# Kernel tuning notes

Hardware: AMD Instinct MI355X
Metric: run time of the kernel (lower is better)

Reference implementation:

```python
import jax, jax.numpy as jnp
import numpy as np

FH = FW = 3

def _decomp_layer(x, f0, f1, f2, f3):
    # x: (B, C, H, W); f0: (F, r), f1: (FH, r), f2: (FW, r), f3: (C, r)
    B, C, H, W = x.shape
    Ho, Wo = H - FH + 1, W - FW + 1
    # unfold -> patches (B, C, Ho, Wo, FH, FW); fixed 3x3 loop, not a data-dim loop
    patches = jnp.stack(
        [jnp.stack([x[:, :, i:i + Ho, j:j + Wo] for j in range(FW)], axis=-1)
         for i in range(FH)], axis=-2)
    # permute to (B, Ho, Wo, FH, FW, C) as in torch's permute(0,2,3,4,5,1)
    patches = patches.transpose(0, 2, 3, 4, 5, 1)
    # CP contraction: collapse fh, fw, c against rank factors, then expand to filters
    t = jnp.einsum('bhwxyc,xr,yr,cr->bhwr', patches, f1, f2, f3)
    return jnp.einsum('bhwr,fr->bfhw', t, f0)  # (B, F, Ho, Wo)


def setup_inputs() -> dict:
    key = jax.random.key(0)
    ks = jax.random.split(key, 12)
    B, C, H, W = 512, 3, 32, 32
    F, R, NC = 32, 16, 10
    s = 0.1
    return {
        'x': jax.random.normal(ks[0], (B, C, H, W), jnp.float32),
        'l1_f0': jax.random.normal(ks[1], (F, R), jnp.float32) * s,
        'l1_f1': jax.random.normal(ks[2], (FH, R), jnp.float32) * s,
        'l1_f2': jax.random.normal(ks[3], (FW, R), jnp.float32) * s,
        'l1_f3': jax.random.normal(ks[4], (C, R), jnp.float32) * s,
        'l2_f0': jax.random.normal(ks[5], (F, R), jnp.float32) * s,
        'l2_f1': jax.random.normal(ks[6], (FH, R), jnp.float32) * s,
        'l2_f2': jax.random.normal(ks[7], (FW, R), jnp.float32) * s,
        'l2_f3': jax.random.normal(ks[8], (F, R), jnp.float32) * s,
        'W_cls': jax.random.normal(ks[9], (NC, 25088), jnp.float32) * 0.01,
        'b_cls': jnp.zeros((NC,), jnp.float32),
    }


def reference(x, l1_f0, l1_f1, l1_f2, l1_f3, l2_f0, l2_f1, l2_f2, l2_f3, W_cls, b_cls):
    h = _decomp_layer(x, l1_f0, l1_f1, l1_f2, l1_f3)        # (B, 32, 30, 30)
    h = _decomp_layer(h, l2_f0, l2_f1, l2_f2, l2_f3)        # (B, 32, 28, 28)
    h = h.reshape(h.shape[0], -1)                            # (B, 25088)
    logits = h @ W_cls.T + b_cls
    return jax.nn.log_softmax(logits, axis=1)
```

## Files before the change

### kernel.cpp

```cpp
#include <hip/hip_runtime.h>
#include <math.h>


__global__ __launch_bounds__(256) void precomp1(
    const float* __restrict__ l1_f0, const float* __restrict__ l1_f1,
    const float* __restrict__ l1_f2, const float* __restrict__ l1_f3,
    const float* __restrict__ l2_f0, const float* __restrict__ l2_f1,
    const float* __restrict__ l2_f2, const float* __restrict__ l2_f3,
    const float* __restrict__ Wcls,
    float* __restrict__ Wc3, float* __restrict__ Kc) {
    __shared__ float sWc2[784];
    __shared__ float sM[256];
    const int tid = threadIdx.x;
    const int blk = blockIdx.x;

    if (blk < 160) {
        const int n = blk >> 4, r2 = blk & 15;
        for (int q = tid; q < 784; q += 256) {
            float acc = 0.f;
#pragma unroll
            for (int f = 0; f < 32; ++f)
                acc += l2_f0[f * 16 + r2] * Wcls[n * 25088 + f * 784 + q];
            sWc2[q] = acc;
        }
        __syncthreads();
        float cw[9];
#pragma unroll
        for (int ij = 0; ij < 9; ++ij) {
            int i = ij / 3, j = ij - (ij / 3) * 3;
            cw[ij] = l2_f1[i * 16 + r2] * l2_f2[j * 16 + r2];
        }
        for (int p = tid; p < 900; p += 256) {
            int h = p / 30, w = p - (p / 30) * 30;
            float acc = 0.f;
#pragma unroll
            for (int i = 0; i < 3; ++i) {
                int hh = h - i;
                if (hh < 0 || hh > 27) continue;
#pragma unroll
                for (int j = 0; j < 3; ++j) {
                    int ww = w - j;
                    if (ww < 0 || ww > 27) continue;
                    acc += cw[i * 3 + j] * sWc2[hh * 28 + ww];
                }
            }
            Wc3[blk * 900 + p] = acc;
        }
    } else {
        {
            int r1 = tid >> 4, r2 = tid & 15;
            float acc = 0.f;
#pragma unroll
            for (int f = 0; f < 32; ++f)
                acc += l1_f0[f * 16 + r1] * l2_f3[f * 16 + r2];
            sM[tid] = acc;
        }
        __syncthreads();
        for (int t = tid; t < 432; t += 256) {
            int c = t / 144;
            int rem = t - c * 144;
            int ij = rem >> 4;
            int r2 = rem & 15;
            int i = ij / 3, j = ij - i * 3;
            float acc = 0.f;
#pragma unroll
            for (int r1 = 0; r1 < 16; ++r1) {
                float cw1v = l1_f1[i * 16 + r1] * l1_f2[j * 16 + r1];
                acc += l1_f3[c * 16 + r1] * cw1v * sM[r1 * 16 + r2];
            }
            Kc[t] = acc;
        }
    }
}

__global__ __launch_bounds__(256) void precomp2(
    const float* __restrict__ Wc3, const float* __restrict__ Kc,
    float* __restrict__ Wx) {
    const int t = blockIdx.x * 256 + threadIdx.x;
    if (t >= 30720) return;
    const int n = t / 3072;
    const int rem = t - n * 3072;
    const int c = rem >> 10;
    const int p = rem & 1023;
    const int H = p >> 5, W = p & 31;
    const float* wn = Wc3 + n * 14400;
    float acc = 0.f;
#pragma unroll
    for (int i = 0; i < 3; ++i) {
        int hh = H - i;
        if (hh < 0 || hh >= 30) continue;
#pragma unroll
        for (int j = 0; j < 3; ++j) {
            int ww = W - j;
            if (ww < 0 || ww >= 30) continue;
            const float* wp = wn + hh * 30 + ww;
            const float* kp = Kc + (c * 9 + i * 3 + j) * 16;
#pragma unroll
            for (int r2 = 0; r2 < 16; ++r2)
                acc += kp[r2] * wp[r2 * 900];
        }
    }
    Wx[t] = acc;
}

__global__ __launch_bounds__(256) void cls_kernel(
    const float* __restrict__ x, const float* __restrict__ Wx,
    const float* __restrict__ b_cls, float* __restrict__ out) {
    __shared__ float sred[4][10];
    __shared__ float slog[10];
    const int tid = threadIdx.x;
    const int b = blockIdx.x;
    const float4* xb = (const float4*)(x + b * 3072);
    const float4* wx4 = (const float4*)Wx;

    float acc[10];
#pragma unroll
    for (int n = 0; n < 10; ++n) acc[n] = 0.f;
#pragma unroll
    for (int k = 0; k < 3; ++k) {
        const int idx = tid + k * 256;
        float4 xv = xb[idx];
#pragma unroll
        for (int n = 0; n < 10; ++n) {
            float4 wv = wx4[n * 768 + idx];
            acc[n] += xv.x * wv.x + xv.y * wv.y + xv.z * wv.z + xv.w * wv.w;
        }
    }

    const int lane = tid & 63, wid = tid >> 6;
#pragma unroll
    for (int n = 0; n < 10; ++n) {
        float v = acc[n];
        for (int off = 32; off > 0; off >>= 1)
            v += __shfl_down(v, off, 64);
        if (lane == 0) sred[wid][n] = v;
    }
    __syncthreads();
    if (tid < 10) {
        slog[tid] = b_cls[tid] + sred[0][tid] + sred[1][tid]
                  + sred[2][tid] + sred[3][tid];
    }
    __syncthreads();
    if (tid < 10) {
        float m = -1e30f;
#pragma unroll
        for (int n = 0; n < 10; ++n) m = fmaxf(m, slog[n]);
        float ssum = 0.f;
#pragma unroll
        for (int n = 0; n < 10; ++n) ssum += expf(slog[n] - m);
        out[b * 10 + tid] = slog[tid] - m - logf(ssum);
    }
}

extern "C" void kernel_launch(void* const* d_in, const int* in_sizes, int n_in,
                              void* d_out, int out_size, void* d_ws, size_t ws_size,
                              hipStream_t stream) {
    const float* x     = (const float*)d_in[0];
    const float* l1_f0 = (const float*)d_in[1];
    const float* l1_f1 = (const float*)d_in[2];
    const float* l1_f2 = (const float*)d_in[3];
    const float* l1_f3 = (const float*)d_in[4];
    const float* l2_f0 = (const float*)d_in[5];
    const float* l2_f1 = (const float*)d_in[6];
    const float* l2_f2 = (const float*)d_in[7];
    const float* l2_f3 = (const float*)d_in[8];
    const float* Wcls  = (const float*)d_in[9];
    const float* bcls  = (const float*)d_in[10];
    float* out = (float*)d_out;

    float* Wc3 = (float*)d_ws;
    float* Kc  = Wc3 + 144000;
    float* Wx  = Kc + 432;

    precomp1<<<dim3(161), dim3(256), 0, stream>>>(
        l1_f0, l1_f1, l1_f2, l1_f3, l2_f0, l2_f1, l2_f2, l2_f3, Wcls, Wc3, Kc);
    precomp2<<<dim3(120), dim3(256), 0, stream>>>(Wc3, Kc, Wx);
    cls_kernel<<<dim3(512), dim3(256), 0, stream>>>(x, Wx, bcls, out);
}
```

Baseline: 93.04 us.

## Fold both conv layers into a combined 5x5 kernel and merge precompute kernels

Replaces the two precompute kernels with one. Each block redundantly builds the composed layer1∘layer2 weight tensor G (C×5×5×F) in shared memory, then correlates W_cls directly with that 5x5 kernel to produce Wx. This removes one kernel launch and the global round trip through the Wc3 and Kc intermediates. In exchange every block recomputes the small factor products, and each output now does 25×32 taps instead of 9×16.

```diff
diff --git a/kernel.cpp b/kernel.cpp
--- a/kernel.cpp
+++ b/kernel.cpp
@@ -2,102 +2,92 @@
 #include <math.h>
 
 
-__global__ __launch_bounds__(256) void precomp1(
+__global__ __launch_bounds__(256) void wx_kernel(
     const float* __restrict__ l1_f0, const float* __restrict__ l1_f1,
     const float* __restrict__ l1_f2, const float* __restrict__ l1_f3,
     const float* __restrict__ l2_f0, const float* __restrict__ l2_f1,
     const float* __restrict__ l2_f2, const float* __restrict__ l2_f3,
     const float* __restrict__ Wcls,
-    float* __restrict__ Wc3, float* __restrict__ Kc) {
-    __shared__ float sWc2[784];
+    float* __restrict__ Wx) {
     __shared__ float sM[256];
+    __shared__ float sK[432];
+    __shared__ float sE[1200];
+    __shared__ float sG[2400];
     const int tid = threadIdx.x;
-    const int blk = blockIdx.x;
 
-    if (blk < 160) {
-        const int n = blk >> 4, r2 = blk & 15;
-        for (int q = tid; q < 784; q += 256) {
-            float acc = 0.f;
+    {
+        int r1 = tid >> 4, r2 = tid & 15;
+        float acc = 0.f;
 #pragma unroll
-            for (int f = 0; f < 32; ++f)
-                acc += l2_f0[f * 16 + r2] * Wcls[n * 25088 + f * 784 + q];
-            sWc2[q] = acc;
+        for (int f = 0; f < 32; ++f)
+            acc += l1_f0[f * 16 + r1] * l2_f3[f * 16 + r2];
+        sM[tid] = acc;
+    }
+    __syncthreads();
+    for (int t = tid; t < 432; t += 256) {
+        int r2 = t & 15;
+        int e = t >> 4;
+        int c = e / 9, ij = e - c * 9;
+        int i = ij / 3, j = ij - i * 3;
+        float acc = 0.f;
+#pragma unroll
+        for (int r1 = 0; r1 < 16; ++r1)
+            acc += l1_f3[c * 16 + r1] * l1_f1[i * 16 + r1] * l1_f2[j * 16 + r1]
+                 * sM[r1 * 16 + r2];
+        sK[t] = acc;
+    }
+    __syncthreads();
+    for (int t = tid; t < 1200; t += 256) {
+        int r2 = t & 15;
+        int e = t >> 4;
+        int c = e / 25, uv = e - c * 25;
+        int u = uv / 5, v = uv - u * 5;
+        float acc = 0.f;
+        int ilo = u > 2 ? u - 2 : 0, ihi = u < 2 ? u : 2;
+        int jlo = v > 2 ? v - 2 : 0, jhi = v < 2 ? v : 2;
+        for (int i = ilo; i <= ihi; ++i) {
+            int k = u - i;
+            for (int j = jlo; j <= jhi; ++j) {
+                int l = v - j;
+                acc += sK[(c * 9 + i * 3 + j) * 16 + r2]
+                     * l2_f1[k * 16 + r2] * l2_f2[l * 16 + r2];
+            }
         }
-        __syncthreads();
-        float cw[9];
+        sE[t] = acc;
+    }
+    __syncthreads();
+    for (int t = tid; t < 2400; t += 256) {
+        int f = t & 31;
+        int e = t >> 5;
+        float acc = 0.f;
 #pragma unroll
-        for (int ij = 0; ij < 9; ++ij) {
-            int i = ij / 3, j = ij - (ij / 3) * 3;
-            cw[ij] = l2_f1[i * 16 + r2] * l2_f2[j * 16 + r2];
-        }
-        for (int p = tid; p < 900; p += 256) {
-            int h = p / 30, w = p - (p / 30) * 30;
-            float acc = 0.f;
-#pragma unroll
-            for (int i = 0; i < 3; ++i) {
-                int hh = h - i;
-                if (hh < 0 || hh > 27) continue;
-#pragma unroll
-                for (int j = 0; j < 3; ++j) {
-                    int ww = w - j;
-                    if (ww < 0 || ww > 27) continue;
-                    acc += cw[i * 3 + j] * sWc2[hh * 28 + ww];
-                }
-            }
-            Wc3[blk * 900 + p] = acc;
-        }
-    } else {
-        {
-            int r1 = tid >> 4, r2 = tid & 15;
-            float acc = 0.f;
-#pragma unroll
-            for (int f = 0; f < 32; ++f)
-                acc += l1_f0[f * 16 + r1] * l2_f3[f * 16 + r2];
-            sM[tid] = acc;
-        }
-        __syncthreads();
-        for (int t = tid; t < 432; t += 256) {
-            int c = t / 144;
-            int rem = t - c * 144;
-            int ij = rem >> 4;
-            int r2 = rem & 15;
-            int i = ij / 3, j = ij - i * 3;
-            float acc = 0.f;
-#pragma unroll
-            for (int r1 = 0; r1 < 16; ++r1) {
-                float cw1v = l1_f1[i * 16 + r1] * l1_f2[j * 16 + r1];
-                acc += l1_f3[c * 16 + r1] * cw1v * sM[r1 * 16 + r2];
-            }
-            Kc[t] = acc;
-        }
+        for (int r2 = 0; r2 < 16; ++r2)
+            acc += sE[e * 16 + r2] * l2_f0[f * 16 + r2];
+        sG[t] = acc;
     }
-}
+    __syncthreads();
 
-__global__ __launch_bounds__(256) void precomp2(
-    const float* __restrict__ Wc3, const float* __restrict__ Kc,
-    float* __restrict__ Wx) {
-    const int t = blockIdx.x * 256 + threadIdx.x;
-    if (t >= 30720) return;
+    const int t = blockIdx.x * 256 + tid;
     const int n = t / 3072;
     const int rem = t - n * 3072;
     const int c = rem >> 10;
     const int p = rem & 1023;
     const int H = p >> 5, W = p & 31;
-    const float* wn = Wc3 + n * 14400;
+    const float* wn = Wcls + n * 25088;
     float acc = 0.f;
 #pragma unroll
-    for (int i = 0; i < 3; ++i) {
-        int hh = H - i;
-        if (hh < 0 || hh >= 30) continue;
+    for (int u = 0; u < 5; ++u) {
+        int hh = H - u;
+        if (hh < 0 || hh >= 28) continue;
 #pragma unroll
-        for (int j = 0; j < 3; ++j) {
-            int ww = W - j;
-            if (ww < 0 || ww >= 30) continue;
-            const float* wp = wn + hh * 30 + ww;
-            const float* kp = Kc + (c * 9 + i * 3 + j) * 16;
+        for (int v = 0; v < 5; ++v) {
+            int ww = W - v;
+            if (ww < 0 || ww >= 28) continue;
+            const float* wp = wn + hh * 28 + ww;
+            const float* gp = &sG[(c * 25 + u * 5 + v) * 32];
 #pragma unroll
-            for (int r2 = 0; r2 < 16; ++r2)
-                acc += kp[r2] * wp[r2 * 900];
+            for (int f = 0; f < 32; ++f)
+                acc += gp[f] * wp[f * 784];
         }
     }
     Wx[t] = acc;
@@ -168,12 +158,9 @@
     const float* bcls  = (const float*)d_in[10];
     float* out = (float*)d_out;
 
-    float* Wc3 = (float*)d_ws;
-    float* Kc  = Wc3 + 144000;
-    float* Wx  = Kc + 432;
+    float* Wx = (float*)d_ws;
 
-    precomp1<<<dim3(161), dim3(256), 0, stream>>>(
-        l1_f0, l1_f1, l1_f2, l1_f3, l2_f0, l2_f1, l2_f2, l2_f3, Wcls, Wc3, Kc);
-    precomp2<<<dim3(120), dim3(256), 0, stream>>>(Wc3, Kc, Wx);
+    wx_kernel<<<dim3(120), dim3(256), 0, stream>>>(
+        l1_f0, l1_f1, l1_f2, l1_f3, l2_f0, l2_f1, l2_f2, l2_f3, Wcls, Wx);
     cls_kernel<<<dim3(512), dim3(256), 0, stream>>>(x, Wx, bcls, out);
 }
```

New measurement: 100.8 us. +8.3%, slower.
